# Kernel optimization log

Hardware: AMD Instinct MI355X
Metric: run time of the kernel (lower is better)

Reference implementation:

```python
import jax, jax.numpy as jnp
import numpy as np
import math

HEAD = 4
B, N, C = 8, 1024, 256


def setup_inputs() -> dict:
    key = jax.random.key(0)
    k1, k2, k3, k4, k5 = jax.random.split(key, 5)
    query = jax.random.normal(k1, (B, N, C), dtype=jnp.float32)
    keyt = jax.random.normal(k2, (B, N, C), dtype=jnp.float32)
    value = jax.random.normal(k3, (B, N, C), dtype=jnp.float32)
    mask = jax.random.randint(k4, (B, N, N), 0, 2).astype(bool)
    dis = jax.random.normal(k5, (B, N, N), dtype=jnp.float32)
    return {"query": query, "key": keyt, "value": value, "mask": mask, "dis": dis}


def reference(query, key, value, mask, dis):
    Bq, Nq, Cq = key.shape
    d = Cq // HEAD
    # split heads: [B,N,C] -> [h,B,N,d]
    q = query.reshape(Bq, Nq, HEAD, d).transpose(2, 0, 1, 3)
    k = key.reshape(Bq, Nq, HEAD, d).transpose(2, 0, 1, 3)
    v = value.reshape(Bq, Nq, HEAD, d).transpose(2, 0, 1, 3)
    # scores: [h,B,N,N]; note: dis added BEFORE scaling, as in the torch code
    scores = jnp.einsum('hbnd,hbmd->hbnm', q, k)
    scores = scores + dis[None]            # dis broadcasts over head dim
    scores = scores / math.sqrt(d)
    scores = jnp.where(mask[None], -jnp.inf, scores)
    p_attn = jax.nn.softmax(scores, axis=-1)
    out = jnp.einsum('hbnm,hbmd->hbnd', p_attn, v)  # [h,B,N,d]
    out = out.transpose(1, 2, 0, 3).reshape(Bq, Nq, Cq)
    return out, p_attn
```

## Files before the change

kernel.cpp:

```cpp
#include <hip/hip_runtime.h>
#include <math.h>

#define HEADS 4
#define BATCH 8
#define SEQ   1024
#define CH    256
#define DH    64
#define RB    16
#define NTHR  512
#define SSTR  1032

typedef float  floatx4  __attribute__((ext_vector_type(4)));
typedef float  floatx2  __attribute__((ext_vector_type(2)));
typedef short  shortx8  __attribute__((ext_vector_type(8)));
typedef short  shortx4  __attribute__((ext_vector_type(4)));

__device__ __forceinline__ unsigned short f2bf(float f) {
    unsigned u = __float_as_uint(f);
    unsigned r = u + 0x7FFFu + ((u >> 16) & 1u);
    return (unsigned short)(r >> 16);
}
__device__ __forceinline__ float bf2f(unsigned short h) {
    return __uint_as_float(((unsigned)h) << 16);
}
__device__ __forceinline__ shortx8 pack8(float4 a, float4 b) {
    shortx8 r;
    r[0] = (short)f2bf(a.x); r[1] = (short)f2bf(a.y);
    r[2] = (short)f2bf(a.z); r[3] = (short)f2bf(a.w);
    r[4] = (short)f2bf(b.x); r[5] = (short)f2bf(b.y);
    r[6] = (short)f2bf(b.z); r[7] = (short)f2bf(b.w);
    return r;
}

__global__ __launch_bounds__(256)
void prep(const float* __restrict__ q, const float* __restrict__ k,
          const float* __restrict__ v, const void* __restrict__ maskp,
          unsigned short* __restrict__ qb, unsigned short* __restrict__ kb,
          unsigned short* __restrict__ vt, unsigned* __restrict__ pm)
{
    __shared__ unsigned short tl[64][68];
    const int t = threadIdx.x;
    const int bid = blockIdx.x;
    if (bid < 2048) {
        const float* src = (bid < 1024) ? q : k;
        unsigned short* dst = (bid < 1024) ? qb : kb;
        size_t idx = (size_t)(bid & 1023) * 2048 + (size_t)t * 8;
        float4 a = *(const float4*)(src + idx);
        float4 b = *(const float4*)(src + idx + 4);
        *(shortx8*)(dst + idx) = pack8(a, b);
        return;
    }
    if (bid < 2560) {
        const int vb = bid - 2048;
        const int nt = vb & 15, h = (vb >> 4) & 3, b = vb >> 6;
        const int n0 = nt * 64;
        const float* vsrc = v + ((size_t)(b * SEQ + n0)) * CH + h * DH;
        #pragma unroll
        for (int it = 0; it < 4; ++it) {
            int fid = it * 256 + t;
            int n = fid >> 4, cc = (fid & 15) * 4;
            float4 x = *(const float4*)(vsrc + (size_t)n * CH + cc);
            tl[n][cc]     = f2bf(x.x);
            tl[n][cc + 1] = f2bf(x.y);
            tl[n][cc + 2] = f2bf(x.z);
            tl[n][cc + 3] = f2bf(x.w);
        }
        __syncthreads();
        unsigned short* vout = vt + ((size_t)((b * HEADS + h) * DH)) * SEQ + n0;
        #pragma unroll
        for (int it = 0; it < 2; ++it) {
            int cid = it * 256 + t;
            int d = cid >> 3, nc = cid & 7;
            shortx8 r;
            #pragma unroll
            for (int j = 0; j < 8; ++j) r[j] = (short)tl[nc * 8 + j][d];
            *(shortx8*)(vout + (size_t)d * SEQ + nc * 8) = r;
        }
        return;
    }
    const int vb2 = bid - 2560;
    const int b = vb2 >> 7, rg = vb2 & 127;
    const int sub = t >> 5, wq = t & 31;
    const int row = rg * 8 + sub;
    const int w_ = wq >> 2, qd_ = wq & 3;
    int fl;
    {
        const unsigned* mw = (const unsigned*)maskp;
        const int lane = t & 63;
        int found = 0;
        #pragma unroll
        for (int j = 0; j < 16; ++j)
            if (mw[lane * 16 + j] & 0xFFFFFF00u) found = 1;
        fl = (__ballot(found != 0) != 0ULL) ? 1 : 0;
    }
    const unsigned char* m8  = (const unsigned char*)maskp;
    const int*           m32 = (const int*)maskp;
    unsigned u = 0;
    #pragma unroll
    for (int mc = 0; mc < 8; ++mc) {
        #pragma unroll
        for (int r = 0; r < 4; ++r) {
            size_t idx = ((size_t)(b * SEQ + row)) * SEQ
                       + mc * 128 + w_ * 16 + qd_ * 4 + r;
            int mk = fl ? (int)m8[idx] : m32[idx];
            u |= (mk ? 1u : 0u) << (mc * 4 + r);
        }
    }
    pm[(((size_t)b * SEQ + row) << 5) + wq] = u;
}

__global__ __launch_bounds__(NTHR)
void attn_mfma(const unsigned short* __restrict__ qb,
               const unsigned short* __restrict__ kbf,
               const unsigned short* __restrict__ vt,
               const unsigned* __restrict__ pm,
               const float* __restrict__ dis, float* __restrict__ out,
               float* __restrict__ pout)
{
    __shared__ unsigned short Sraw[RB][SSTR];
    __shared__ float Opart[RB][65];
    __shared__ float invs[RB];
    __shared__ float wmax[8][16];
    __shared__ float wsum[8][16];

    const int t   = threadIdx.x;
    const int bid = blockIdx.x;
    const int b   = bid & (BATCH - 1);
    const int h   = (bid >> 3) & (HEADS - 1);
    const int n0  = (bid >> 5) * RB;

    const int lane = t & 63;
    const int w    = t >> 6;
    const int ln   = lane & 15;
    const int qd   = lane >> 4;

    const unsigned mb = pm[(((size_t)b * SEQ + n0 + ln) << 5) + w * 4 + qd];

    const unsigned short* qrow = qb + ((size_t)(b * SEQ + n0 + ln)) * CH + h * DH;
    shortx8 aq0 = *(const shortx8*)(qrow + qd * 8);
    shortx8 aq1 = *(const shortx8*)(qrow + 32 + qd * 8);

    const unsigned short* kbase = kbf + ((size_t)(b * SEQ)) * CH + h * DH;
    const unsigned short* vbase = vt + ((size_t)((b * HEADS + h) * DH)) * SEQ;
    const float* disrow =
        dis + ((size_t)(b * SEQ + n0 + ln)) * SEQ + w * 16 + qd * 4;

    float s[32];
    #pragma unroll
    for (int mc = 0; mc < 8; ++mc) {
        const int mgb = mc * 128 + w * 16;
        const unsigned short* krow = kbase + (size_t)(mgb + ln) * CH;
        shortx8 kf0 = *(const shortx8*)(krow + qd * 8);
        shortx8 kf1 = *(const shortx8*)(krow + 32 + qd * 8);
        float4 dv = *(const float4*)(disrow + mc * 128);
        floatx4 acc = {0.f, 0.f, 0.f, 0.f};
        acc = __builtin_amdgcn_mfma_f32_16x16x32_bf16(kf0, aq0, acc, 0, 0, 0);
        acc = __builtin_amdgcn_mfma_f32_16x16x32_bf16(kf1, aq1, acc, 0, 0, 0);
        s[mc*4+0] = ((mb >> (mc*4+0)) & 1u) ? -INFINITY : (acc[0] + dv.x) * 0.125f;
        s[mc*4+1] = ((mb >> (mc*4+1)) & 1u) ? -INFINITY : (acc[1] + dv.y) * 0.125f;
        s[mc*4+2] = ((mb >> (mc*4+2)) & 1u) ? -INFINITY : (acc[2] + dv.z) * 0.125f;
        s[mc*4+3] = ((mb >> (mc*4+3)) & 1u) ? -INFINITY : (acc[3] + dv.w) * 0.125f;
    }

    float mx = s[0];
    #pragma unroll
    for (int i = 1; i < 32; ++i) mx = fmaxf(mx, s[i]);
    mx = fmaxf(mx, __shfl_xor(mx, 16));
    mx = fmaxf(mx, __shfl_xor(mx, 32));
    if (qd == 0) wmax[w][ln] = mx;
    __syncthreads();
    #pragma unroll
    for (int j = 0; j < 8; ++j) mx = fmaxf(mx, wmax[j][ln]);

    float sum = 0.f;
    #pragma unroll
    for (int i = 0; i < 32; ++i) {
        float x = __expf(s[i] - mx);
        s[i] = x;
        sum += x;
    }
    sum += __shfl_xor(sum, 16);
    sum += __shfl_xor(sum, 32);
    if (qd == 0) wsum[w][ln] = sum;
    __syncthreads();
    float tot = 0.f;
    #pragma unroll
    for (int j = 0; j < 8; ++j) tot += wsum[j][ln];
    const float inv = 1.0f / tot;
    if (w == 0 && qd == 0) invs[ln] = inv;

    float* prow = pout + ((size_t)((h * BATCH + b) * SEQ + n0 + ln)) * SEQ
                + w * 16 + qd * 4;
    #pragma unroll
    for (int mc = 0; mc < 8; ++mc) {
        shortx4 ev;
        ev[0] = (short)f2bf(s[mc*4+0]);
        ev[1] = (short)f2bf(s[mc*4+1]);
        ev[2] = (short)f2bf(s[mc*4+2]);
        ev[3] = (short)f2bf(s[mc*4+3]);
        *(shortx4*)&Sraw[ln][mc * 128 + w * 16 + qd * 4] = ev;
        float4 pv = { s[mc*4+0] * inv, s[mc*4+1] * inv,
                      s[mc*4+2] * inv, s[mc*4+3] * inv };
        *(float4*)(prow + mc * 128) = pv;
    }
    __syncthreads();

    const int hm = w >> 2;
    const int c  = (w & 3) * 16;
    floatx4 accA = {0.f, 0.f, 0.f, 0.f};
    floatx4 accB = {0.f, 0.f, 0.f, 0.f};
    const unsigned short* vcol = vbase + (size_t)(c + ln) * SEQ;
    #pragma unroll 4
    for (int it = 0; it < 16; it += 2) {
        const int kk0 = hm * 512 + (it >> 1) * 64 + qd * 8;
        const int kk1 = kk0 + 32;
        shortx8 af0  = *(const shortx8*)&Sraw[ln][kk0];
        shortx8 bf0  = *(const shortx8*)(vcol + kk0);
        shortx8 af1  = *(const shortx8*)&Sraw[ln][kk1];
        shortx8 bf1  = *(const shortx8*)(vcol + kk1);
        accA = __builtin_amdgcn_mfma_f32_16x16x32_bf16(af0, bf0, accA, 0, 0, 0);
        accB = __builtin_amdgcn_mfma_f32_16x16x32_bf16(af1, bf1, accB, 0, 0, 0);
    }
    floatx4 acco;
    acco[0] = accA[0] + accB[0];
    acco[1] = accA[1] + accB[1];
    acco[2] = accA[2] + accB[2];
    acco[3] = accA[3] + accB[3];

    if (hm == 1) {
        #pragma unroll
        for (int r = 0; r < 4; ++r) Opart[qd * 4 + r][c + ln] = acco[r];
    }
    __syncthreads();
    if (hm == 0) {
        #pragma unroll
        for (int r = 0; r < 4; ++r) {
            int row = qd * 4 + r;
            float ov = (acco[r] + Opart[row][c + ln]) * invs[row];
            out[((size_t)(b * SEQ + n0 + row)) * CH + h * DH + c + ln] = ov;
        }
    }
}

extern "C" void kernel_launch(void* const* d_in, const int* in_sizes, int n_in,
                              void* d_out, int out_size, void* d_ws, size_t ws_size,
                              hipStream_t stream) {
    const float* q    = (const float*)d_in[0];
    const float* k    = (const float*)d_in[1];
    const float* v    = (const float*)d_in[2];
    const void*  mask = d_in[3];
    const float* dis  = (const float*)d_in[4];
    float* out  = (float*)d_out;
    float* pout = out + (size_t)BATCH * SEQ * CH;

    unsigned short* qb  = (unsigned short*)d_ws;
    unsigned short* kbw = qb  + (size_t)BATCH * SEQ * CH;
    unsigned short* vtw = kbw + (size_t)BATCH * SEQ * CH;
    unsigned*       pmw = (unsigned*)(vtw + (size_t)BATCH * SEQ * CH);
    (void)ws_size;

    prep<<<3584, 256, 0, stream>>>(q, k, v, mask, qb, kbw, vtw, pmw);
    attn_mfma<<<HEADS * BATCH * (SEQ / RB), NTHR, 0, stream>>>(
        qb, kbw, vtw, pmw, dis, out, pout);
}
```

Before: 297.0 us.

## Replace block-wide softmax with single-wave two-pass recompute kernel

```diff
diff --git a/kernel.cpp b/kernel.cpp
--- a/kernel.cpp
+++ b/kernel.cpp
@@ -7,11 +7,8 @@
 #define CH    256
 #define DH    64
 #define RB    16
-#define NTHR  512
-#define SSTR  1032
 
 typedef float  floatx4  __attribute__((ext_vector_type(4)));
-typedef float  floatx2  __attribute__((ext_vector_type(2)));
 typedef short  shortx8  __attribute__((ext_vector_type(8)));
 typedef short  shortx4  __attribute__((ext_vector_type(4)));
 
@@ -19,9 +16,6 @@
     unsigned u = __float_as_uint(f);
     unsigned r = u + 0x7FFFu + ((u >> 16) & 1u);
     return (unsigned short)(r >> 16);
-}
-__device__ __forceinline__ float bf2f(unsigned short h) {
-    return __uint_as_float(((unsigned)h) << 16);
 }
 __device__ __forceinline__ shortx8 pack8(float4 a, float4 b) {
     shortx8 r;
@@ -44,9 +38,12 @@
     if (bid < 2048) {
         const float* src = (bid < 1024) ? q : k;
         unsigned short* dst = (bid < 1024) ? qb : kb;
+        const float sc = (bid < 1024) ? 0.125f : 1.0f;
         size_t idx = (size_t)(bid & 1023) * 2048 + (size_t)t * 8;
         float4 a = *(const float4*)(src + idx);
         float4 b = *(const float4*)(src + idx + 4);
+        a.x *= sc; a.y *= sc; a.z *= sc; a.w *= sc;
+        b.x *= sc; b.y *= sc; b.z *= sc; b.w *= sc;
         *(shortx8*)(dst + idx) = pack8(a, b);
         return;
     }
@@ -109,32 +106,23 @@
     pm[(((size_t)b * SEQ + row) << 5) + wq] = u;
 }
 
-__global__ __launch_bounds__(NTHR)
-void attn_mfma(const unsigned short* __restrict__ qb,
+__global__ __launch_bounds__(64)
+void attn_wave(const unsigned short* __restrict__ qb,
                const unsigned short* __restrict__ kbf,
                const unsigned short* __restrict__ vt,
                const unsigned* __restrict__ pm,
                const float* __restrict__ dis, float* __restrict__ out,
                float* __restrict__ pout)
 {
-    __shared__ unsigned short Sraw[RB][SSTR];
-    __shared__ float Opart[RB][65];
-    __shared__ float invs[RB];
-    __shared__ float wmax[8][16];
-    __shared__ float wsum[8][16];
+    __shared__ unsigned short ps[2][16][40];
 
     const int t   = threadIdx.x;
     const int bid = blockIdx.x;
     const int b   = bid & (BATCH - 1);
     const int h   = (bid >> 3) & (HEADS - 1);
     const int n0  = (bid >> 5) * RB;
-
-    const int lane = t & 63;
-    const int w    = t >> 6;
-    const int ln   = lane & 15;
-    const int qd   = lane >> 4;
-
-    const unsigned mb = pm[(((size_t)b * SEQ + n0 + ln) << 5) + w * 4 + qd];
+    const int ln  = t & 15;
+    const int qd  = t >> 4;
 
     const unsigned short* qrow = qb + ((size_t)(b * SEQ + n0 + ln)) * CH + h * DH;
     shortx8 aq0 = *(const shortx8*)(qrow + qd * 8);
@@ -143,102 +131,110 @@
     const unsigned short* kbase = kbf + ((size_t)(b * SEQ)) * CH + h * DH;
     const unsigned short* vbase = vt + ((size_t)((b * HEADS + h) * DH)) * SEQ;
     const float* disrow =
-        dis + ((size_t)(b * SEQ + n0 + ln)) * SEQ + w * 16 + qd * 4;
-
-    float s[32];
-    #pragma unroll
-    for (int mc = 0; mc < 8; ++mc) {
-        const int mgb = mc * 128 + w * 16;
-        const unsigned short* krow = kbase + (size_t)(mgb + ln) * CH;
-        shortx8 kf0 = *(const shortx8*)(krow + qd * 8);
-        shortx8 kf1 = *(const shortx8*)(krow + 32 + qd * 8);
-        float4 dv = *(const float4*)(disrow + mc * 128);
-        floatx4 acc = {0.f, 0.f, 0.f, 0.f};
-        acc = __builtin_amdgcn_mfma_f32_16x16x32_bf16(kf0, aq0, acc, 0, 0, 0);
-        acc = __builtin_amdgcn_mfma_f32_16x16x32_bf16(kf1, aq1, acc, 0, 0, 0);
-        s[mc*4+0] = ((mb >> (mc*4+0)) & 1u) ? -INFINITY : (acc[0] + dv.x) * 0.125f;
-        s[mc*4+1] = ((mb >> (mc*4+1)) & 1u) ? -INFINITY : (acc[1] + dv.y) * 0.125f;
-        s[mc*4+2] = ((mb >> (mc*4+2)) & 1u) ? -INFINITY : (acc[2] + dv.z) * 0.125f;
-        s[mc*4+3] = ((mb >> (mc*4+3)) & 1u) ? -INFINITY : (acc[3] + dv.w) * 0.125f;
-    }
-
-    float mx = s[0];
-    #pragma unroll
-    for (int i = 1; i < 32; ++i) mx = fmaxf(mx, s[i]);
-    mx = fmaxf(mx, __shfl_xor(mx, 16));
-    mx = fmaxf(mx, __shfl_xor(mx, 32));
-    if (qd == 0) wmax[w][ln] = mx;
-    __syncthreads();
-    #pragma unroll
-    for (int j = 0; j < 8; ++j) mx = fmaxf(mx, wmax[j][ln]);
+        dis + ((size_t)(b * SEQ + n0 + ln)) * SEQ + qd * 4;
+    const unsigned* pmrow = pm + (((size_t)(b * SEQ + n0 + ln)) << 5) + qd;
 
     float sum = 0.f;
-    #pragma unroll
-    for (int i = 0; i < 32; ++i) {
-        float x = __expf(s[i] - mx);
-        s[i] = x;
-        sum += x;
+    for (int wg = 0; wg < 8; ++wg) {
+        const unsigned mw = pmrow[wg * 4];
+        #pragma unroll 4
+        for (int mc = 0; mc < 8; ++mc) {
+            const int cb = mc * 128 + wg * 16;
+            const unsigned short* krow = kbase + (size_t)(cb + ln) * CH;
+            shortx8 kf0 = *(const shortx8*)(krow + qd * 8);
+            shortx8 kf1 = *(const shortx8*)(krow + 32 + qd * 8);
+            float4 dv = *(const float4*)(disrow + cb);
+            floatx4 acc = {0.f, 0.f, 0.f, 0.f};
+            acc = __builtin_amdgcn_mfma_f32_16x16x32_bf16(kf0, aq0, acc, 0, 0, 0);
+            acc = __builtin_amdgcn_mfma_f32_16x16x32_bf16(kf1, aq1, acc, 0, 0, 0);
+            float x0 = __expf(fmaf(dv.x, 0.125f, acc[0]));
+            float x1 = __expf(fmaf(dv.y, 0.125f, acc[1]));
+            float x2 = __expf(fmaf(dv.z, 0.125f, acc[2]));
+            float x3 = __expf(fmaf(dv.w, 0.125f, acc[3]));
+            if ((mw >> (mc * 4 + 0)) & 1u) x0 = 0.f;
+            if ((mw >> (mc * 4 + 1)) & 1u) x1 = 0.f;
+            if ((mw >> (mc * 4 + 2)) & 1u) x2 = 0.f;
+            if ((mw >> (mc * 4 + 3)) & 1u) x3 = 0.f;
+            sum += x0 + x1 + x2 + x3;
+        }
     }
     sum += __shfl_xor(sum, 16);
     sum += __shfl_xor(sum, 32);
-    if (qd == 0) wsum[w][ln] = sum;
-    __syncthreads();
-    float tot = 0.f;
+    const float inv = 1.0f / sum;
+
+    floatx4 o0 = {0.f,0.f,0.f,0.f}, o1 = {0.f,0.f,0.f,0.f};
+    floatx4 o2 = {0.f,0.f,0.f,0.f}, o3 = {0.f,0.f,0.f,0.f};
+    float* prow = pout + ((size_t)((h * BATCH + b) * SEQ + n0 + ln)) * SEQ
+                + qd * 4;
+    int par = 0;
+    for (int wp = 0; wp < 4; ++wp) {
+        const unsigned mw0 = pmrow[(2 * wp) * 4];
+        const unsigned mw1 = pmrow[(2 * wp + 1) * 4];
+        #pragma unroll 2
+        for (int mc = 0; mc < 8; ++mc) {
+            const int cb = mc * 128 + wp * 32;
+            const unsigned short* vk = vbase + cb + qd * 8;
+            shortx8 vf0 = *(const shortx8*)(vk + (size_t)(0 * 16 + ln) * SEQ);
+            shortx8 vf1 = *(const shortx8*)(vk + (size_t)(1 * 16 + ln) * SEQ);
+            shortx8 vf2 = *(const shortx8*)(vk + (size_t)(2 * 16 + ln) * SEQ);
+            shortx8 vf3 = *(const shortx8*)(vk + (size_t)(3 * 16 + ln) * SEQ);
+            const unsigned short* kr0 = kbase + (size_t)(cb + ln) * CH;
+            const unsigned short* kr1 = kbase + (size_t)(cb + 16 + ln) * CH;
+            shortx8 k00 = *(const shortx8*)(kr0 + qd * 8);
+            shortx8 k01 = *(const shortx8*)(kr0 + 32 + qd * 8);
+            shortx8 k10 = *(const shortx8*)(kr1 + qd * 8);
+            shortx8 k11 = *(const shortx8*)(kr1 + 32 + qd * 8);
+            float4 dv0 = *(const float4*)(disrow + cb);
+            float4 dv1 = *(const float4*)(disrow + cb + 16);
+            floatx4 a0 = {0.f,0.f,0.f,0.f}, a1 = {0.f,0.f,0.f,0.f};
+            a0 = __builtin_amdgcn_mfma_f32_16x16x32_bf16(k00, aq0, a0, 0, 0, 0);
+            a0 = __builtin_amdgcn_mfma_f32_16x16x32_bf16(k01, aq1, a0, 0, 0, 0);
+            a1 = __builtin_amdgcn_mfma_f32_16x16x32_bf16(k10, aq0, a1, 0, 0, 0);
+            a1 = __builtin_amdgcn_mfma_f32_16x16x32_bf16(k11, aq1, a1, 0, 0, 0);
+            float p0[4], p1[4];
+            #pragma unroll
+            for (int r = 0; r < 4; ++r) {
+                float e0 = __expf(fmaf(((const float*)&dv0)[r], 0.125f, a0[r]));
+                float e1 = __expf(fmaf(((const float*)&dv1)[r], 0.125f, a1[r]));
+                if ((mw0 >> (mc * 4 + r)) & 1u) e0 = 0.f;
+                if ((mw1 >> (mc * 4 + r)) & 1u) e1 = 0.f;
+                p0[r] = e0; p1[r] = e1;
+            }
+            float4 pv0 = { p0[0]*inv, p0[1]*inv, p0[2]*inv, p0[3]*inv };
+            float4 pv1 = { p1[0]*inv, p1[1]*inv, p1[2]*inv, p1[3]*inv };
+            *(float4*)(prow + cb)      = pv0;
+            *(float4*)(prow + cb + 16) = pv1;
+            shortx4 e0, e1;
+            e0[0] = (short)f2bf(p0[0]); e0[1] = (short)f2bf(p0[1]);
+            e0[2] = (short)f2bf(p0[2]); e0[3] = (short)f2bf(p0[3]);
+            e1[0] = (short)f2bf(p1[0]); e1[1] = (short)f2bf(p1[1]);
+            e1[2] = (short)f2bf(p1[2]); e1[3] = (short)f2bf(p1[3]);
+            *(shortx4*)&ps[par][ln][qd * 4]      = e0;
+            *(shortx4*)&ps[par][ln][16 + qd * 4] = e1;
+            __syncthreads();
+            shortx8 af = *(const shortx8*)&ps[par][ln][qd * 8];
+            o0 = __builtin_amdgcn_mfma_f32_16x16x32_bf16(af, vf0, o0, 0, 0, 0);
+            o1 = __builtin_amdgcn_mfma_f32_16x16x32_bf16(af, vf1, o1, 0, 0, 0);
+            o2 = __builtin_amdgcn_mfma_f32_16x16x32_bf16(af, vf2, o2, 0, 0, 0);
+            o3 = __builtin_amdgcn_mfma_f32_16x16x32_bf16(af, vf3, o3, 0, 0, 0);
+            par ^= 1;
+        }
+    }
+
+    const float invq0 = __shfl(inv, qd * 4 + 0);
+    const float invq1 = __shfl(inv, qd * 4 + 1);
+    const float invq2 = __shfl(inv, qd * 4 + 2);
+    const float invq3 = __shfl(inv, qd * 4 + 3);
     #pragma unroll
-    for (int j = 0; j < 8; ++j) tot += wsum[j][ln];
-    const float inv = 1.0f / tot;
-    if (w == 0 && qd == 0) invs[ln] = inv;
-
-    float* prow = pout + ((size_t)((h * BATCH + b) * SEQ + n0 + ln)) * SEQ
-                + w * 16 + qd * 4;
-    #pragma unroll
-    for (int mc = 0; mc < 8; ++mc) {
-        shortx4 ev;
-        ev[0] = (short)f2bf(s[mc*4+0]);
-        ev[1] = (short)f2bf(s[mc*4+1]);
-        ev[2] = (short)f2bf(s[mc*4+2]);
-        ev[3] = (short)f2bf(s[mc*4+3]);
-        *(shortx4*)&Sraw[ln][mc * 128 + w * 16 + qd * 4] = ev;
-        float4 pv = { s[mc*4+0] * inv, s[mc*4+1] * inv,
-                      s[mc*4+2] * inv, s[mc*4+3] * inv };
-        *(float4*)(prow + mc * 128) = pv;
-    }
-    __syncthreads();
-
-    const int hm = w >> 2;
-    const int c  = (w & 3) * 16;
-    floatx4 accA = {0.f, 0.f, 0.f, 0.f};
-    floatx4 accB = {0.f, 0.f, 0.f, 0.f};
-    const unsigned short* vcol = vbase + (size_t)(c + ln) * SEQ;
-    #pragma unroll 4
-    for (int it = 0; it < 16; it += 2) {
-        const int kk0 = hm * 512 + (it >> 1) * 64 + qd * 8;
-        const int kk1 = kk0 + 32;
-        shortx8 af0  = *(const shortx8*)&Sraw[ln][kk0];
-        shortx8 bf0  = *(const shortx8*)(vcol + kk0);
-        shortx8 af1  = *(const shortx8*)&Sraw[ln][kk1];
-        shortx8 bf1  = *(const shortx8*)(vcol + kk1);
-        accA = __builtin_amdgcn_mfma_f32_16x16x32_bf16(af0, bf0, accA, 0, 0, 0);
-        accB = __builtin_amdgcn_mfma_f32_16x16x32_bf16(af1, bf1, accB, 0, 0, 0);
-    }
-    floatx4 acco;
-    acco[0] = accA[0] + accB[0];
-    acco[1] = accA[1] + accB[1];
-    acco[2] = accA[2] + accB[2];
-    acco[3] = accA[3] + accB[3];
-
-    if (hm == 1) {
-        #pragma unroll
-        for (int r = 0; r < 4; ++r) Opart[qd * 4 + r][c + ln] = acco[r];
-    }
-    __syncthreads();
-    if (hm == 0) {
-        #pragma unroll
-        for (int r = 0; r < 4; ++r) {
-            int row = qd * 4 + r;
-            float ov = (acco[r] + Opart[row][c + ln]) * invs[row];
-            out[((size_t)(b * SEQ + n0 + row)) * CH + h * DH + c + ln] = ov;
-        }
+    for (int dr = 0; dr < 4; ++dr) {
+        const float iq = (dr == 0) ? invq0 : (dr == 1) ? invq1
+                       : (dr == 2) ? invq2 : invq3;
+        float* orow = out + ((size_t)(b * SEQ + n0 + qd * 4 + dr)) * CH
+                    + h * DH + ln;
+        orow[0]  = o0[dr] * iq;
+        orow[16] = o1[dr] * iq;
+        orow[32] = o2[dr] * iq;
+        orow[48] = o3[dr] * iq;
     }
 }
 
@@ -260,6 +256,6 @@
     (void)ws_size;
 
     prep<<<3584, 256, 0, stream>>>(q, k, v, mask, qb, kbw, vtw, pmw);
-    attn_mfma<<<HEADS * BATCH * (SEQ / RB), NTHR, 0, stream>>>(
+    attn_wave<<<HEADS * BATCH * (SEQ / RB), 64, 0, stream>>>(
         qb, kbw, vtw, pmw, dis, out, pout);
 }
```

Result: slower. 322.1 us (+8.4%).
